# Performance work log

Hardware: AMD Instinct MI355X
Metric: run time of the kernel (lower is better)

The kernel has to match this reference:

```python
import jax, jax.numpy as jnp
import numpy as np

T = 4
TAU = 2.0
THR = 0.2
N_NODES = 50000
N_EDGES = 400000
N_LINKS = 50000
N_FEAT = 256
ENC0, ENC1 = 256, 128
DEC = 64


def _make_spike(grad_fn):
    @jax.custom_vjp
    def spike(v):
        return (v >= 0).astype(v.dtype)

    def fwd(v):
        return (v >= 0).astype(v.dtype), v

    def bwd(res, g):
        return (g * grad_fn(res),)

    spike.defvjp(fwd, bwd)
    return spike


def _sg_sigmoid(x, alpha=4.0):
    s = jax.nn.sigmoid(alpha * x)
    return alpha * s * (1.0 - s)


def _sg_pwl(x, w=0.5, c=0.0):
    return jnp.where(jnp.abs(x) < w, 1.0 / w, c)


spike_sig = _make_spike(_sg_sigmoid)   # default LIFNode surrogate (Sigmoid, alpha=4)
spike_pwl = _make_spike(_sg_pwl)       # PiecewiseLeakyReLU(w=0.5, c=0.0)


def _lif(v, x, spike_fn):
    # decay_input=False, v_reset=None -> soft reset, decay toward 0
    v = v * (1.0 - 1.0 / TAU) + x
    s = spike_fn(v - THR)
    return v - s * THR, s


def setup_inputs() -> dict:
    key = jax.random.key(0)
    ks = jax.random.split(key, 12)
    x = jax.random.uniform(ks[0], (N_NODES, N_FEAT), jnp.float32)
    edge_src = jax.random.randint(ks[1], (N_EDGES,), 0, N_NODES, jnp.int32)
    edge_dst = jax.random.randint(ks[2], (N_EDGES,), 0, N_NODES, jnp.int32)
    edge_w = jax.random.uniform(ks[3], (N_EDGES,), jnp.float32)
    nodes_s = jax.random.randint(ks[4], (N_LINKS,), 0, N_NODES, jnp.int32)
    nodes_t = jax.random.randint(ks[5], (N_LINKS,), 0, N_NODES, jnp.int32)
    W1 = jax.random.normal(ks[6], (N_FEAT, ENC0), jnp.float32) / np.sqrt(N_FEAT)
    W2 = jax.random.normal(ks[7], (N_FEAT + ENC0, ENC1), jnp.float32) / np.sqrt(N_FEAT + ENC0)
    Wd = jax.random.normal(ks[8], (ENC1, DEC), jnp.float32) / np.sqrt(ENC1)
    bd = jax.random.normal(ks[9], (DEC,), jnp.float32) * 0.01
    w_rec = jax.random.normal(ks[10], (DEC,), jnp.float32)
    return {"x": x, "W1": W1, "W2": W2, "Wd": Wd, "bd": bd, "w_rec": w_rec,
            "edge_w": edge_w, "edge_src": edge_src, "edge_dst": edge_dst,
            "nodes_s": nodes_s, "nodes_t": nodes_t}


def reference(x, W1, W2, Wd, bd, w_rec, edge_w, edge_src, edge_dst, nodes_s, nodes_t):
    N = x.shape[0]
    L = nodes_s.shape[0]
    key = jax.random.key(42)
    ew = edge_w[:, None]

    def propagate(feat):  # sparse adj @ feat via edge-list scatter-add
        return jax.ops.segment_sum(feat[edge_src] * ew, edge_dst, num_segments=N)

    def poisson(v, k):  # PoissonEncoder: spike ~ Bernoulli(v), zero gradient
        u = jax.random.uniform(k, v.shape, v.dtype)
        return (u <= jax.lax.stop_gradient(v)).astype(v.dtype)

    carry0 = (jnp.zeros((N, ENC0), x.dtype),              # v of layer0 z-LIF
              jnp.zeros((N, N_FEAT + ENC0), x.dtype),      # v of layer1 h-LIF
              jnp.zeros((N, ENC1), x.dtype),               # v of layer1 z-LIF
              jnp.zeros((2 * L, DEC), x.dtype))            # v of decoder LIF

    def step(carry, t):
        v0z, v1h, v1z, vdec = carry
        kt = jax.random.fold_in(key, t)
        k1, k2 = jax.random.split(kt)
        inp = poisson(x, k1)                    # inputs_encoding(x)
        h0 = propagate(inp)                     # layer0 GraphConvolution
        hs0 = poisson(h0, k2)                   # layer0 PoissonEncoder
        v0z, zs0 = _lif(v0z, hs0 @ W1, spike_pwl)
        inp1 = jnp.concatenate([zs0, hs0], axis=1)  # [N, 512]
        h1 = propagate(inp1)                    # layer1 GraphConvolution
        v1h, hs1 = _lif(v1h, h1, spike_sig)     # layer1 LIFNode (default surrogate)
        v1z, zs1 = _lif(v1z, hs1 @ W2, spike_pwl)
        hcat = jnp.concatenate([zs1[nodes_s], zs1[nodes_t]], axis=0)  # [2L, 128]
        vdec, zd = _lif(vdec, hcat @ Wd + bd, spike_pwl)
        y_t = jnp.sum(zd[:L] * w_rec * zd[L:], axis=1)  # WeightedInnerProduct_Link
        return (v0z, v1h, v1z, vdec), y_t

    _, y = jax.lax.scan(step, carry0, jnp.arange(T))  # y: [T, L]
    return jax.nn.sigmoid(jnp.mean(y, axis=0))        # PotentialOutput readout + sigmoid
```

## Files before the change

kernel.cpp:

```cpp
#include <hip/hip_runtime.h>
#include <stdint.h>
#include <math.h>

#define NN    50000
#define NE    400000
#define NL    50000
#define TOT   12800000

#define JAX_PARTITIONABLE 1

struct K8 { uint32_t a[4]; uint32_t b[4]; };

__host__ __device__ inline uint32_t rotl32(uint32_t x, int r){ return (x<<r)|(x>>(32-r)); }

__host__ __device__ inline void tf2x32(uint32_t k0, uint32_t k1, uint32_t x0, uint32_t x1,
                                       uint32_t &o0, uint32_t &o1) {
  uint32_t k2 = k0 ^ k1 ^ 0x1BD11BDAu;
  x0 += k0; x1 += k1;
#define TFR(r) { x0 += x1; x1 = rotl32(x1,(r)); x1 ^= x0; }
  TFR(13) TFR(15) TFR(26) TFR(6)
  x0 += k1; x1 += k2 + 1u;
  TFR(17) TFR(29) TFR(16) TFR(24)
  x0 += k2; x1 += k0 + 2u;
  TFR(13) TFR(15) TFR(26) TFR(6)
  x0 += k0; x1 += k1 + 3u;
  TFR(17) TFR(29) TFR(16) TFR(24)
  x0 += k1; x1 += k2 + 4u;
  TFR(13) TFR(15) TFR(26) TFR(6)
  x0 += k2; x1 += k0 + 5u;
#undef TFR
  o0 = x0; o1 = x1;
}

__device__ inline float u01(uint32_t b){
  return __uint_as_float((b>>9) | 0x3f800000u) - 1.0f;
}

__device__ inline uint32_t jax_bits32(uint32_t ka, uint32_t kb, uint32_t i, uint32_t total){
#if JAX_PARTITIONABLE
  uint32_t o0,o1; tf2x32(ka,kb, 0u, i, o0,o1); return o0^o1;
#else
  uint32_t h = total>>1; uint32_t o0,o1;
  if (i < h){ tf2x32(ka,kb, i, i+h, o0,o1); return o0; }
  else      { tf2x32(ka,kb, i-h, i, o0,o1); return o1; }
#endif
}

__device__ inline double shflxor_d(double x, int m){
  union { double d; int i[2]; } u; u.d = x;
  u.i[0] = __shfl_xor(u.i[0], m, 64);
  u.i[1] = __shfl_xor(u.i[1], m, 64);
  return u.d;
}

__device__ inline bool lif32(float &v, float a){
  v = __fadd_rn(__fmul_rn(v, 0.5f), a);
  float d = __fsub_rn(v, 0.2f);
  bool s = (d >= 0.0f);
  v = s ? d : v;
  return s;
}

#define FORCE_V(x) asm volatile("" : "+v"(x))

__device__ inline float bitmaskf(uint32_t w, int b, float wr){
#if __has_builtin(__builtin_amdgcn_sbfe)
  int m = __builtin_amdgcn_sbfe((int)w, b, 1);
#else
  int m = ((int)(w << (31-b))) >> 31;
#endif
  return __int_as_float(__float_as_int(wr) & m);
}

__global__ __launch_bounds__(256) void k_hist(const int* __restrict__ dst, int* __restrict__ cnt){
  int e = blockIdx.x*256 + threadIdx.x;
  if (e < NE) atomicAdd(&cnt[dst[e]], 1);
}

__global__ __launch_bounds__(1024) void k_scan(const int* __restrict__ cnt,
    int* __restrict__ rp, int* __restrict__ cur){
  __shared__ int buf[1024];
  __shared__ int carry;
  int tid = threadIdx.x;
  if (tid==0) carry = 0;
  __syncthreads();
  for (int base=0; base<NN; base+=1024){
    int v = (base+tid < NN) ? cnt[base+tid] : 0;
    buf[tid] = v; __syncthreads();
    for (int off=1; off<1024; off<<=1){
      int t = (tid>=off) ? buf[tid-off] : 0;
      __syncthreads();
      buf[tid] += t;
      __syncthreads();
    }
    int excl = buf[tid] - v + carry;
    if (base+tid < NN){ rp[base+tid] = excl; cur[base+tid] = excl; }
    __syncthreads();
    if (tid==0) carry += buf[1023];
    __syncthreads();
  }
  if (tid==0) rp[NN] = NE;
}

__global__ __launch_bounds__(256) void k_scatter(const int* __restrict__ dst,
    int* __restrict__ cur, int* __restrict__ eidx){
  int e = blockIdx.x*256 + threadIdx.x;
  if (e < NE){ int p = atomicAdd(&cur[dst[e]], 1); eidx[p] = e; }
}

__global__ __launch_bounds__(256) void k_sortrow(const int* __restrict__ rp,
    int* __restrict__ eidx, const int* __restrict__ esrc, const float* __restrict__ ew,
    int* __restrict__ csrc, float* __restrict__ cw){
  int n = blockIdx.x*256 + threadIdx.x;
  if (n >= NN) return;
  int lo = rp[n], hi = rp[n+1];
  for (int a=lo+1; a<hi; a++){
    int k = eidx[a]; int b = a-1;
    while (b>=lo && eidx[b]>k){ eidx[b+1]=eidx[b]; b--; }
    eidx[b+1] = k;
  }
  for (int p=lo; p<hi; p++){ int e = eidx[p]; csrc[p] = esrc[e]; cw[p] = ew[e]; }
}


__global__ __launch_bounds__(256) void k_pois_x(const float* __restrict__ x,
    uint64_t* __restrict__ bits, K8 K){
  int n = blockIdx.x, f = threadIdx.x;
  uint32_t i = (uint32_t)n*256u + (uint32_t)f;
  float xv = x[i];
  uint64_t pack[4];
  #pragma unroll
  for (int t=0;t<4;t++){
    bool b = (u01(jax_bits32(K.a[t],K.b[t], i, TOT)) <= xv);
    pack[t] = __ballot(b);
  }
  if ((f & 63)==0){
    uint64_t* dst = bits + ((size_t)n*4 + (f>>6))*4;
    #pragma unroll
    for (int t=0;t<4;t++) dst[t] = pack[t];
  }
}

__global__ __launch_bounds__(256) void k_h0(const int* __restrict__ rp,
    const int* __restrict__ csrc, const float* __restrict__ cw,
    const uint64_t* __restrict__ inb, uint64_t* __restrict__ outb, K8 K){
  int n = blockIdx.x, f = threadIdx.x;
  int wi = f>>6, sh = f&63;
  int lo = rp[n], hi = rp[n+1];
  float a[4] = {0.f,0.f,0.f,0.f};
  for (int p=lo;p<hi;p++){
    int s = csrc[p]; float w = cw[p];
    const uint64_t* bp = inb + ((size_t)s*4 + wi)*4;
    uint64_t w0=bp[0], w1=bp[1], w2=bp[2], w3=bp[3];
    a[0] = __fadd_rn(a[0], ((w0>>sh)&1ull) ? w : 0.0f);
    a[1] = __fadd_rn(a[1], ((w1>>sh)&1ull) ? w : 0.0f);
    a[2] = __fadd_rn(a[2], ((w2>>sh)&1ull) ? w : 0.0f);
    a[3] = __fadd_rn(a[3], ((w3>>sh)&1ull) ? w : 0.0f);
  }
  uint32_t i = (uint32_t)n*256u + (uint32_t)f;
  uint64_t pack[4];
  #pragma unroll
  for (int t=0;t<4;t++){
    bool b = (u01(jax_bits32(K.a[t],K.b[t], i, TOT)) <= a[t]);
    pack[t] = __ballot(b);
  }
  if (sh==0){
    uint64_t* dst = outb + ((size_t)n*4 + wi)*4;
    #pragma unroll
    for (int t=0;t<4;t++) dst[t] = pack[t];
  }
}

__global__ __launch_bounds__(256) void k_z0(const uint64_t* __restrict__ inb,
    const float* __restrict__ W, uint64_t* __restrict__ outb){
  __shared__ __align__(16) float sp[4*64*4];
  __shared__ uint64_t wbuf[16];
  int j = threadIdx.x;
  int n0 = blockIdx.x*4;
  float acc[4][4];
  #pragma unroll
  for (int t=0;t<4;t++)
    #pragma unroll
    for (int i=0;i<4;i++) acc[t][i] = 0.0f;

  for (int kt=0; kt<4; kt++){
    if (j < 16) wbuf[j] = inb[(((size_t)(n0+(j>>2)))*4 + kt)*4 + (j&3)];
    __syncthreads();
    {
      int i = j>>6, k = j&63;
      uint64_t w0=wbuf[i*4+0], w1=wbuf[i*4+1], w2=wbuf[i*4+2], w3=wbuf[i*4+3];
      float4 f;
      f.x = ((w0>>k)&1ull) ? 1.0f : 0.0f;
      f.y = ((w1>>k)&1ull) ? 1.0f : 0.0f;
      f.z = ((w2>>k)&1ull) ? 1.0f : 0.0f;
      f.w = ((w3>>k)&1ull) ? 1.0f : 0.0f;
      *(float4*)&sp[(i*64+k)*4] = f;
    }
    __syncthreads();
    const float* Wp = W + (size_t)(kt*64)*256 + j;
    #pragma unroll 4
    for (int q=0;q<64;q++){
      float wr = Wp[(size_t)q*256];
      float4 s0 = *(const float4*)&sp[(0*64+q)*4];
      float4 s1 = *(const float4*)&sp[(1*64+q)*4];
      float4 s2 = *(const float4*)&sp[(2*64+q)*4];
      float4 s3 = *(const float4*)&sp[(3*64+q)*4];
      acc[0][0]=__fmaf_rn(s0.x,wr,acc[0][0]); acc[1][0]=__fmaf_rn(s0.y,wr,acc[1][0]);
      acc[2][0]=__fmaf_rn(s0.z,wr,acc[2][0]); acc[3][0]=__fmaf_rn(s0.w,wr,acc[3][0]);
      acc[0][1]=__fmaf_rn(s1.x,wr,acc[0][1]); acc[1][1]=__fmaf_rn(s1.y,wr,acc[1][1]);
      acc[2][1]=__fmaf_rn(s1.z,wr,acc[2][1]); acc[3][1]=__fmaf_rn(s1.w,wr,acc[3][1]);
      acc[0][2]=__fmaf_rn(s2.x,wr,acc[0][2]); acc[1][2]=__fmaf_rn(s2.y,wr,acc[1][2]);
      acc[2][2]=__fmaf_rn(s2.z,wr,acc[2][2]); acc[3][2]=__fmaf_rn(s2.w,wr,acc[3][2]);
      acc[0][3]=__fmaf_rn(s3.x,wr,acc[0][3]); acc[1][3]=__fmaf_rn(s3.y,wr,acc[1][3]);
      acc[2][3]=__fmaf_rn(s3.z,wr,acc[2][3]); acc[3][3]=__fmaf_rn(s3.w,wr,acc[3][3]);
    }
    __syncthreads();
  }

  int wi = j>>6;
  #pragma unroll
  for (int i=0;i<4;i++){
    float v = 0.0f;
    uint64_t pack[4];
    #pragma unroll
    for (int t=0;t<4;t++){
      bool s = lif32(v, acc[t][i]);
      pack[t] = __ballot(s);
    }
    if ((j&63)==0){
      uint64_t* dst = outb + (((size_t)(n0+i))*4 + wi)*4;
      #pragma unroll
      for (int t=0;t<4;t++) dst[t] = pack[t];
    }
  }
}

__global__ __launch_bounds__(512) void k_h1(const int* __restrict__ rp,
    const int* __restrict__ csrc, const float* __restrict__ cw,
    const uint64_t* __restrict__ zs0b, const uint64_t* __restrict__ hs0b,
    uint64_t* __restrict__ hs1b){
  int n = blockIdx.x, f = threadIdx.x;
  int wi = f>>6, sh = f&63;
  const uint64_t* plane = (wi<4) ? zs0b : hs0b;
  int wo = wi & 3;
  int lo = rp[n], hi = rp[n+1];
  float a[4] = {0.f,0.f,0.f,0.f};
  for (int p=lo;p<hi;p++){
    int s = csrc[p]; float w = cw[p];
    const uint64_t* bp = plane + ((size_t)s*4 + wo)*4;
    uint64_t w0=bp[0], w1=bp[1], w2=bp[2], w3=bp[3];
    a[0] = __fadd_rn(a[0], ((w0>>sh)&1ull) ? w : 0.0f);
    a[1] = __fadd_rn(a[1], ((w1>>sh)&1ull) ? w : 0.0f);
    a[2] = __fadd_rn(a[2], ((w2>>sh)&1ull) ? w : 0.0f);
    a[3] = __fadd_rn(a[3], ((w3>>sh)&1ull) ? w : 0.0f);
  }
  float v = 0.0f;
  uint64_t pack[4];
  #pragma unroll
  for (int t=0;t<4;t++){
    bool s = lif32(v, a[t]);
    pack[t] = __ballot(s);
  }
  if (sh==0){
    uint64_t* dst = hs1b + ((size_t)n*8 + wi)*4;
    #pragma unroll
    for (int t=0;t<4;t++) dst[t] = pack[t];
  }
}

__global__ __launch_bounds__(128) void k_z1(const uint64_t* __restrict__ inb,
    const float* __restrict__ W, uint64_t* __restrict__ outb){
  __shared__ __align__(16) float sp[4*64*4];
  __shared__ uint64_t wbuf[16];
  int j = threadIdx.x;
  int n0 = blockIdx.x*4;
  float acc[4][4];
  #pragma unroll
  for (int t=0;t<4;t++)
    #pragma unroll
    for (int i=0;i<4;i++) acc[t][i] = 0.0f;

  for (int kt=0; kt<8; kt++){
    if (j < 16) wbuf[j] = inb[(((size_t)(n0+(j>>2)))*8 + kt)*4 + (j&3)];
    __syncthreads();
    #pragma unroll
    for (int rep=0; rep<2; rep++){
      int idx = rep*128 + j;
      int i = idx>>6, k = idx&63;
      uint64_t w0=wbuf[i*4+0], w1=wbuf[i*4+1], w2=wbuf[i*4+2], w3=wbuf[i*4+3];
      float4 f;
      f.x = ((w0>>k)&1ull) ? 1.0f : 0.0f;
      f.y = ((w1>>k)&1ull) ? 1.0f : 0.0f;
      f.z = ((w2>>k)&1ull) ? 1.0f : 0.0f;
      f.w = ((w3>>k)&1ull) ? 1.0f : 0.0f;
      *(float4*)&sp[(i*64+k)*4] = f;
    }
    __syncthreads();
    const float* Wp = W + (size_t)(kt*64)*128 + j;
    #pragma unroll 4
    for (int q=0;q<64;q++){
      float wr = Wp[(size_t)q*128];
      float4 s0 = *(const float4*)&sp[(0*64+q)*4];
      float4 s1 = *(const float4*)&sp[(1*64+q)*4];
      float4 s2 = *(const float4*)&sp[(2*64+q)*4];
      float4 s3 = *(const float4*)&sp[(3*64+q)*4];
      acc[0][0]=__fmaf_rn(s0.x,wr,acc[0][0]); acc[1][0]=__fmaf_rn(s0.y,wr,acc[1][0]);
      acc[2][0]=__fmaf_rn(s0.z,wr,acc[2][0]); acc[3][0]=__fmaf_rn(s0.w,wr,acc[3][0]);
      acc[0][1]=__fmaf_rn(s1.x,wr,acc[0][1]); acc[1][1]=__fmaf_rn(s1.y,wr,acc[1][1]);
      acc[2][1]=__fmaf_rn(s1.z,wr,acc[2][1]); acc[3][1]=__fmaf_rn(s1.w,wr,acc[3][1]);
      acc[0][2]=__fmaf_rn(s2.x,wr,acc[0][2]); acc[1][2]=__fmaf_rn(s2.y,wr,acc[1][2]);
      acc[2][2]=__fmaf_rn(s2.z,wr,acc[2][2]); acc[3][2]=__fmaf_rn(s2.w,wr,acc[3][2]);
      acc[0][3]=__fmaf_rn(s3.x,wr,acc[0][3]); acc[1][3]=__fmaf_rn(s3.y,wr,acc[1][3]);
      acc[2][3]=__fmaf_rn(s3.z,wr,acc[2][3]); acc[3][3]=__fmaf_rn(s3.w,wr,acc[3][3]);
    }
    __syncthreads();
  }

  int wi = j>>6;
  #pragma unroll
  for (int i=0;i<4;i++){
    float v = 0.0f;
    uint64_t pack[4];
    #pragma unroll
    for (int t=0;t<4;t++){
      bool s = lif32(v, acc[t][i]);
      pack[t] = __ballot(s);
    }
    if ((j&63)==0){
      uint64_t* dst = outb + (((size_t)(n0+i))*2 + wi)*4;
      #pragma unroll
      for (int t=0;t<4;t++) dst[t] = pack[t];
    }
  }
}

__global__ __launch_bounds__(128) void k_dec_y(const int* __restrict__ ns,
    const int* __restrict__ nt, const uint64_t* __restrict__ zs1b,
    const float* __restrict__ Wd, const float* __restrict__ bd,
    const float* __restrict__ wrec, float* __restrict__ out){
  int i = blockIdx.x;
  int tid = threadIdx.x;
  int row = tid>>6, j = tid&63;
  int node = row ? nt[i] : ns[i];
  float bdj = bd[j];
  double wrecj = (double)wrec[j];
  __shared__ uint64_t sw[2];

  uint32_t wlo[2][4], whi[2][4];
  const uint64_t* bp = zs1b + (size_t)node*8;
  #pragma unroll
  for (int g=0;g<2;g++)
    #pragma unroll
    for (int t=0;t<4;t++){
      uint64_t w8 = bp[g*4+t];
      wlo[g][t] = (uint32_t)w8;
      whi[g][t] = (uint32_t)(w8>>32);
      FORCE_V(wlo[g][t]); FORCE_V(whi[g][t]);
    }

  float acc[4] = {0.f,0.f,0.f,0.f};
  #pragma unroll
  for (int g=0;g<2;g++){
    #pragma unroll
    for (int h=0;h<2;h++){
      #pragma unroll
      for (int c=0;c<2;c++){
        float wr[16];
        #pragma unroll
        for (int q=0;q<16;q++) wr[q] = Wd[(size_t)(g*64+h*32+c*16+q)*64 + j];
        #pragma unroll
        for (int q=0;q<16;q++){
          int b = c*16+q;
          #pragma unroll
          for (int t=0;t<4;t++){
            uint32_t wv = h ? whi[g][t] : wlo[g][t];
            acc[t] = __fadd_rn(acc[t], bitmaskf(wv, b, wr[q]));
          }
        }
      }
    }
  }

  float v = 0.0f;
  double ysum = 0.0;
  #pragma unroll
  for (int t=0;t<4;t++){
    float a = __fadd_rn(acc[t], bdj);
    bool s = lif32(v, a);
    uint64_t bw = __ballot(s);
    if (j==0) sw[row] = bw;
    __syncthreads();
    uint64_t m = sw[0] & sw[1];
    __syncthreads();
    double term = ((m>>j)&1ull) ? wrecj : 0.0;
    #pragma unroll
    for (int off=1; off<64; off<<=1) term += shflxor_d(term, off);
    ysum += term;
  }
  if (tid==0) out[i] = (float)(1.0/(1.0 + exp(-0.25*ysum)));
}

extern "C" void kernel_launch(void* const* d_in, const int* in_sizes, int n_in,
                              void* d_out, int out_size, void* d_ws, size_t ws_size,
                              hipStream_t stream) {
  const float* x    = (const float*)d_in[0];
  const float* W1   = (const float*)d_in[1];
  const float* W2   = (const float*)d_in[2];
  const float* Wd   = (const float*)d_in[3];
  const float* bd   = (const float*)d_in[4];
  const float* wrec = (const float*)d_in[5];
  const float* ew   = (const float*)d_in[6];
  const int* esrc   = (const int*)d_in[7];
  const int* edst   = (const int*)d_in[8];
  const int* ns     = (const int*)d_in[9];
  const int* nt     = (const int*)d_in[10];
  float* out = (float*)d_out;
  (void)in_sizes; (void)n_in; (void)out_size; (void)ws_size;

  char* p = (char*)d_ws;
  uint64_t* inpb = (uint64_t*)p; p += (size_t)NN*16*8;
  uint64_t* hs0b = (uint64_t*)p; p += (size_t)NN*16*8;
  uint64_t* zs0b = (uint64_t*)p; p += (size_t)NN*16*8;
  uint64_t* hs1b = (uint64_t*)p; p += (size_t)NN*32*8;
  uint64_t* zs1b = (uint64_t*)p; p += (size_t)NN*8*8;
  int*   eidx = (int*)p;   p += (size_t)NE*4;
  int*   csrc = (int*)p;   p += (size_t)NE*4;
  float* cw   = (float*)p; p += (size_t)NE*4;
  int*   cnt  = (int*)p;   p += (size_t)(NN+2)*4;
  int*   rp   = (int*)p;   p += (size_t)(NN+2)*4;
  int*   cur  = (int*)p;   p += (size_t)(NN+2)*4;

  K8 K1, K2;
  for (int t=0;t<4;t++){
    uint32_t kt0,kt1;
    tf2x32(0u, 42u, 0u, (uint32_t)t, kt0, kt1);
#if JAX_PARTITIONABLE
    tf2x32(kt0, kt1, 0u, 0u, K1.a[t], K1.b[t]);
    tf2x32(kt0, kt1, 0u, 1u, K2.a[t], K2.b[t]);
#else
    uint32_t A0,B0,A1,B1;
    tf2x32(kt0, kt1, 0u, 2u, A0, B0);
    tf2x32(kt0, kt1, 1u, 3u, A1, B1);
    K1.a[t]=A0; K1.b[t]=A1; K2.a[t]=B0; K2.b[t]=B1;
#endif
  }

  hipMemsetAsync(cnt, 0, (size_t)NN*4, stream);
  k_hist   <<<(NE+255)/256, 256, 0, stream>>>(edst, cnt);
  k_scan   <<<1, 1024, 0, stream>>>(cnt, rp, cur);
  k_scatter<<<(NE+255)/256, 256, 0, stream>>>(edst, cur, eidx);
  k_sortrow<<<(NN+255)/256, 256, 0, stream>>>(rp, eidx, esrc, ew, csrc, cw);

  k_pois_x<<<NN, 256, 0, stream>>>(x, inpb, K1);
  k_h0    <<<NN, 256, 0, stream>>>(rp, csrc, cw, inpb, hs0b, K2);
  k_z0    <<<NN/4, 256, 0, stream>>>(hs0b, W1, zs0b);
  k_h1    <<<NN, 512, 0, stream>>>(rp, csrc, cw, zs0b, hs0b, hs1b);
  k_z1    <<<NN/4, 128, 0, stream>>>(hs1b, W2, zs1b);
  k_dec_y <<<NL, 128, 0, stream>>>(ns, nt, zs1b, Wd, bd, wrec, out);
}
```

Before: 1.739 ms.

## Retile z0/z1 spike GEMMs to eight nodes per block, two columns per thread

The dense spike-times-weight kernels now process eight nodes per block. Each thread computes two output columns for four nodes, so every LDS spike read feeds twice as many FMAs and each weight element is reused across more nodes. The staging step through a small shared word buffer, and the barrier that went with it, is removed: threads read packed bit-words straight from global memory when expanding them to floats. The cost is more accumulator registers per thread and half as many blocks.

Result: faster. 1.633 ms (-6.1%).

```diff
diff --git a/kernel.cpp b/kernel.cpp
--- a/kernel.cpp
+++ b/kernel.cpp
@@ -173,22 +173,26 @@
 
 __global__ __launch_bounds__(256) void k_z0(const uint64_t* __restrict__ inb,
     const float* __restrict__ W, uint64_t* __restrict__ outb){
-  __shared__ __align__(16) float sp[4*64*4];
-  __shared__ uint64_t wbuf[16];
-  int j = threadIdx.x;
-  int n0 = blockIdx.x*4;
-  float acc[4][4];
+  __shared__ __align__(16) float sp[8*64*4];
+  int tid = threadIdx.x;
+  int wave = tid>>6, lane = tid&63;
+  int g = wave>>1;
+  int ch = wave&1;
+  int colBase = ch*128;
+  int n0 = blockIdx.x*8;
+  float acc[4][4][2];
   #pragma unroll
   for (int t=0;t<4;t++)
     #pragma unroll
-    for (int i=0;i<4;i++) acc[t][i] = 0.0f;
+    for (int i=0;i<4;i++){ acc[t][i][0]=0.0f; acc[t][i][1]=0.0f; }
 
   for (int kt=0; kt<4; kt++){
-    if (j < 16) wbuf[j] = inb[(((size_t)(n0+(j>>2)))*4 + kt)*4 + (j&3)];
-    __syncthreads();
-    {
-      int i = j>>6, k = j&63;
-      uint64_t w0=wbuf[i*4+0], w1=wbuf[i*4+1], w2=wbuf[i*4+2], w3=wbuf[i*4+3];
+    #pragma unroll
+    for (int rep=0; rep<2; rep++){
+      int idx = rep*256 + tid;
+      int i = idx>>6, k = idx&63;
+      const uint64_t* bp = inb + (((size_t)(n0+i))*4 + kt)*4;
+      uint64_t w0=bp[0], w1=bp[1], w2=bp[2], w3=bp[3];
       float4 f;
       f.x = ((w0>>k)&1ull) ? 1.0f : 0.0f;
       f.y = ((w1>>k)&1ull) ? 1.0f : 0.0f;
@@ -197,40 +201,52 @@
       *(float4*)&sp[(i*64+k)*4] = f;
     }
     __syncthreads();
-    const float* Wp = W + (size_t)(kt*64)*256 + j;
+    const float* Wrow = W + (size_t)(kt*64)*256 + colBase + lane;
     #pragma unroll 4
     for (int q=0;q<64;q++){
-      float wr = Wp[(size_t)q*256];
-      float4 s0 = *(const float4*)&sp[(0*64+q)*4];
-      float4 s1 = *(const float4*)&sp[(1*64+q)*4];
-      float4 s2 = *(const float4*)&sp[(2*64+q)*4];
-      float4 s3 = *(const float4*)&sp[(3*64+q)*4];
-      acc[0][0]=__fmaf_rn(s0.x,wr,acc[0][0]); acc[1][0]=__fmaf_rn(s0.y,wr,acc[1][0]);
-      acc[2][0]=__fmaf_rn(s0.z,wr,acc[2][0]); acc[3][0]=__fmaf_rn(s0.w,wr,acc[3][0]);
-      acc[0][1]=__fmaf_rn(s1.x,wr,acc[0][1]); acc[1][1]=__fmaf_rn(s1.y,wr,acc[1][1]);
-      acc[2][1]=__fmaf_rn(s1.z,wr,acc[2][1]); acc[3][1]=__fmaf_rn(s1.w,wr,acc[3][1]);
-      acc[0][2]=__fmaf_rn(s2.x,wr,acc[0][2]); acc[1][2]=__fmaf_rn(s2.y,wr,acc[1][2]);
-      acc[2][2]=__fmaf_rn(s2.z,wr,acc[2][2]); acc[3][2]=__fmaf_rn(s2.w,wr,acc[3][2]);
-      acc[0][3]=__fmaf_rn(s3.x,wr,acc[0][3]); acc[1][3]=__fmaf_rn(s3.y,wr,acc[1][3]);
-      acc[2][3]=__fmaf_rn(s3.z,wr,acc[2][3]); acc[3][3]=__fmaf_rn(s3.w,wr,acc[3][3]);
-    }
-    __syncthreads();
-  }
-
-  int wi = j>>6;
+      float wr0 = Wrow[(size_t)q*256];
+      float wr1 = Wrow[(size_t)q*256 + 64];
+      float4 s0 = *(const float4*)&sp[((g*4+0)*64+q)*4];
+      float4 s1 = *(const float4*)&sp[((g*4+1)*64+q)*4];
+      float4 s2 = *(const float4*)&sp[((g*4+2)*64+q)*4];
+      float4 s3 = *(const float4*)&sp[((g*4+3)*64+q)*4];
+      acc[0][0][0]=__fmaf_rn(s0.x,wr0,acc[0][0][0]); acc[0][0][1]=__fmaf_rn(s0.x,wr1,acc[0][0][1]);
+      acc[1][0][0]=__fmaf_rn(s0.y,wr0,acc[1][0][0]); acc[1][0][1]=__fmaf_rn(s0.y,wr1,acc[1][0][1]);
+      acc[2][0][0]=__fmaf_rn(s0.z,wr0,acc[2][0][0]); acc[2][0][1]=__fmaf_rn(s0.z,wr1,acc[2][0][1]);
+      acc[3][0][0]=__fmaf_rn(s0.w,wr0,acc[3][0][0]); acc[3][0][1]=__fmaf_rn(s0.w,wr1,acc[3][0][1]);
+      acc[0][1][0]=__fmaf_rn(s1.x,wr0,acc[0][1][0]); acc[0][1][1]=__fmaf_rn(s1.x,wr1,acc[0][1][1]);
+      acc[1][1][0]=__fmaf_rn(s1.y,wr0,acc[1][1][0]); acc[1][1][1]=__fmaf_rn(s1.y,wr1,acc[1][1][1]);
+      acc[2][1][0]=__fmaf_rn(s1.z,wr0,acc[2][1][0]); acc[2][1][1]=__fmaf_rn(s1.z,wr1,acc[2][1][1]);
+      acc[3][1][0]=__fmaf_rn(s1.w,wr0,acc[3][1][0]); acc[3][1][1]=__fmaf_rn(s1.w,wr1,acc[3][1][1]);
+      acc[0][2][0]=__fmaf_rn(s2.x,wr0,acc[0][2][0]); acc[0][2][1]=__fmaf_rn(s2.x,wr1,acc[0][2][1]);
+      acc[1][2][0]=__fmaf_rn(s2.y,wr0,acc[1][2][0]); acc[1][2][1]=__fmaf_rn(s2.y,wr1,acc[1][2][1]);
+      acc[2][2][0]=__fmaf_rn(s2.z,wr0,acc[2][2][0]); acc[2][2][1]=__fmaf_rn(s2.z,wr1,acc[2][2][1]);
+      acc[3][2][0]=__fmaf_rn(s2.w,wr0,acc[3][2][0]); acc[3][2][1]=__fmaf_rn(s2.w,wr1,acc[3][2][1]);
+      acc[0][3][0]=__fmaf_rn(s3.x,wr0,acc[0][3][0]); acc[0][3][1]=__fmaf_rn(s3.x,wr1,acc[0][3][1]);
+      acc[1][3][0]=__fmaf_rn(s3.y,wr0,acc[1][3][0]); acc[1][3][1]=__fmaf_rn(s3.y,wr1,acc[1][3][1]);
+      acc[2][3][0]=__fmaf_rn(s3.z,wr0,acc[2][3][0]); acc[2][3][1]=__fmaf_rn(s3.z,wr1,acc[2][3][1]);
+      acc[3][3][0]=__fmaf_rn(s3.w,wr0,acc[3][3][0]); acc[3][3][1]=__fmaf_rn(s3.w,wr1,acc[3][3][1]);
+    }
+    __syncthreads();
+  }
+
   #pragma unroll
   for (int i=0;i<4;i++){
-    float v = 0.0f;
-    uint64_t pack[4];
+    int node = n0 + g*4 + i;
+    float v0 = 0.0f, v1 = 0.0f;
+    uint64_t p0[4], p1[4];
     #pragma unroll
     for (int t=0;t<4;t++){
-      bool s = lif32(v, acc[t][i]);
-      pack[t] = __ballot(s);
-    }
-    if ((j&63)==0){
-      uint64_t* dst = outb + (((size_t)(n0+i))*4 + wi)*4;
+      bool s0 = lif32(v0, acc[t][i][0]);
+      bool s1 = lif32(v1, acc[t][i][1]);
+      p0[t] = __ballot(s0);
+      p1[t] = __ballot(s1);
+    }
+    if (lane==0){
+      uint64_t* d0 = outb + ((size_t)node*4 + ch*2    )*4;
+      uint64_t* d1 = outb + ((size_t)node*4 + ch*2 + 1)*4;
       #pragma unroll
-      for (int t=0;t<4;t++) dst[t] = pack[t];
+      for (int t=0;t<4;t++){ d0[t]=p0[t]; d1[t]=p1[t]; }
     }
   }
 }
@@ -270,24 +286,23 @@
 
 __global__ __launch_bounds__(128) void k_z1(const uint64_t* __restrict__ inb,
     const float* __restrict__ W, uint64_t* __restrict__ outb){
-  __shared__ __align__(16) float sp[4*64*4];
-  __shared__ uint64_t wbuf[16];
-  int j = threadIdx.x;
-  int n0 = blockIdx.x*4;
-  float acc[4][4];
+  __shared__ __align__(16) float sp[8*64*4];
+  int tid = threadIdx.x;
+  int g = tid>>6, lane = tid&63;
+  int n0 = blockIdx.x*8;
+  float acc[4][4][2];
   #pragma unroll
   for (int t=0;t<4;t++)
     #pragma unroll
-    for (int i=0;i<4;i++) acc[t][i] = 0.0f;
+    for (int i=0;i<4;i++){ acc[t][i][0]=0.0f; acc[t][i][1]=0.0f; }
 
   for (int kt=0; kt<8; kt++){
-    if (j < 16) wbuf[j] = inb[(((size_t)(n0+(j>>2)))*8 + kt)*4 + (j&3)];
-    __syncthreads();
-    #pragma unroll
-    for (int rep=0; rep<2; rep++){
-      int idx = rep*128 + j;
+    #pragma unroll
+    for (int rep=0; rep<4; rep++){
+      int idx = rep*128 + tid;
       int i = idx>>6, k = idx&63;
-      uint64_t w0=wbuf[i*4+0], w1=wbuf[i*4+1], w2=wbuf[i*4+2], w3=wbuf[i*4+3];
+      const uint64_t* bp = inb + (((size_t)(n0+i))*8 + kt)*4;
+      uint64_t w0=bp[0], w1=bp[1], w2=bp[2], w3=bp[3];
       float4 f;
       f.x = ((w0>>k)&1ull) ? 1.0f : 0.0f;
       f.y = ((w1>>k)&1ull) ? 1.0f : 0.0f;
@@ -296,40 +311,52 @@
       *(float4*)&sp[(i*64+k)*4] = f;
     }
     __syncthreads();
-    const float* Wp = W + (size_t)(kt*64)*128 + j;
+    const float* Wrow = W + (size_t)(kt*64)*128 + lane;
     #pragma unroll 4
     for (int q=0;q<64;q++){
-      float wr = Wp[(size_t)q*128];
-      float4 s0 = *(const float4*)&sp[(0*64+q)*4];
-      float4 s1 = *(const float4*)&sp[(1*64+q)*4];
-      float4 s2 = *(const float4*)&sp[(2*64+q)*4];
-      float4 s3 = *(const float4*)&sp[(3*64+q)*4];
-      acc[0][0]=__fmaf_rn(s0.x,wr,acc[0][0]); acc[1][0]=__fmaf_rn(s0.y,wr,acc[1][0]);
-      acc[2][0]=__fmaf_rn(s0.z,wr,acc[2][0]); acc[3][0]=__fmaf_rn(s0.w,wr,acc[3][0]);
-      acc[0][1]=__fmaf_rn(s1.x,wr,acc[0][1]); acc[1][1]=__fmaf_rn(s1.y,wr,acc[1][1]);
-      acc[2][1]=__fmaf_rn(s1.z,wr,acc[2][1]); acc[3][1]=__fmaf_rn(s1.w,wr,acc[3][1]);
-      acc[0][2]=__fmaf_rn(s2.x,wr,acc[0][2]); acc[1][2]=__fmaf_rn(s2.y,wr,acc[1][2]);
-      acc[2][2]=__fmaf_rn(s2.z,wr,acc[2][2]); acc[3][2]=__fmaf_rn(s2.w,wr,acc[3][2]);
-      acc[0][3]=__fmaf_rn(s3.x,wr,acc[0][3]); acc[1][3]=__fmaf_rn(s3.y,wr,acc[1][3]);
-      acc[2][3]=__fmaf_rn(s3.z,wr,acc[2][3]); acc[3][3]=__fmaf_rn(s3.w,wr,acc[3][3]);
-    }
-    __syncthreads();
-  }
-
-  int wi = j>>6;
+      float wr0 = Wrow[(size_t)q*128];
+      float wr1 = Wrow[(size_t)q*128 + 64];
+      float4 s0 = *(const float4*)&sp[((g*4+0)*64+q)*4];
+      float4 s1 = *(const float4*)&sp[((g*4+1)*64+q)*4];
+      float4 s2 = *(const float4*)&sp[((g*4+2)*64+q)*4];
+      float4 s3 = *(const float4*)&sp[((g*4+3)*64+q)*4];
+      acc[0][0][0]=__fmaf_rn(s0.x,wr0,acc[0][0][0]); acc[0][0][1]=__fmaf_rn(s0.x,wr1,acc[0][0][1]);
+      acc[1][0][0]=__fmaf_rn(s0.y,wr0,acc[1][0][0]); acc[1][0][1]=__fmaf_rn(s0.y,wr1,acc[1][0][1]);
+      acc[2][0][0]=__fmaf_rn(s0.z,wr0,acc[2][0][0]); acc[2][0][1]=__fmaf_rn(s0.z,wr1,acc[2][0][1]);
+      acc[3][0][0]=__fmaf_rn(s0.w,wr0,acc[3][0][0]); acc[3][0][1]=__fmaf_rn(s0.w,wr1,acc[3][0][1]);
+      acc[0][1][0]=__fmaf_rn(s1.x,wr0,acc[0][1][0]); acc[0][1][1]=__fmaf_rn(s1.x,wr1,acc[0][1][1]);
+      acc[1][1][0]=__fmaf_rn(s1.y,wr0,acc[1][1][0]); acc[1][1][1]=__fmaf_rn(s1.y,wr1,acc[1][1][1]);
+      acc[2][1][0]=__fmaf_rn(s1.z,wr0,acc[2][1][0]); acc[2][1][1]=__fmaf_rn(s1.z,wr1,acc[2][1][1]);
+      acc[3][1][0]=__fmaf_rn(s1.w,wr0,acc[3][1][0]); acc[3][1][1]=__fmaf_rn(s1.w,wr1,acc[3][1][1]);
+      acc[0][2][0]=__fmaf_rn(s2.x,wr0,acc[0][2][0]); acc[0][2][1]=__fmaf_rn(s2.x,wr1,acc[0][2][1]);
+      acc[1][2][0]=__fmaf_rn(s2.y,wr0,acc[1][2][0]); acc[1][2][1]=__fmaf_rn(s2.y,wr1,acc[1][2][1]);
+      acc[2][2][0]=__fmaf_rn(s2.z,wr0,acc[2][2][0]); acc[2][2][1]=__fmaf_rn(s2.z,wr1,acc[2][2][1]);
+      acc[3][2][0]=__fmaf_rn(s2.w,wr0,acc[3][2][0]); acc[3][2][1]=__fmaf_rn(s2.w,wr1,acc[3][2][1]);
+      acc[0][3][0]=__fmaf_rn(s3.x,wr0,acc[0][3][0]); acc[0][3][1]=__fmaf_rn(s3.x,wr1,acc[0][3][1]);
+      acc[1][3][0]=__fmaf_rn(s3.y,wr0,acc[1][3][0]); acc[1][3][1]=__fmaf_rn(s3.y,wr1,acc[1][3][1]);
+      acc[2][3][0]=__fmaf_rn(s3.z,wr0,acc[2][3][0]); acc[2][3][1]=__fmaf_rn(s3.z,wr1,acc[2][3][1]);
+      acc[3][3][0]=__fmaf_rn(s3.w,wr0,acc[3][3][0]); acc[3][3][1]=__fmaf_rn(s3.w,wr1,acc[3][3][1]);
+    }
+    __syncthreads();
+  }
+
   #pragma unroll
   for (int i=0;i<4;i++){
-    float v = 0.0f;
-    uint64_t pack[4];
+    int node = n0 + g*4 + i;
+    float v0 = 0.0f, v1 = 0.0f;
+    uint64_t p0[4], p1[4];
     #pragma unroll
     for (int t=0;t<4;t++){
-      bool s = lif32(v, acc[t][i]);
-      pack[t] = __ballot(s);
-    }
-    if ((j&63)==0){
-      uint64_t* dst = outb + (((size_t)(n0+i))*2 + wi)*4;
+      bool s0 = lif32(v0, acc[t][i][0]);
+      bool s1 = lif32(v1, acc[t][i][1]);
+      p0[t] = __ballot(s0);
+      p1[t] = __ballot(s1);
+    }
+    if (lane==0){
+      uint64_t* d0 = outb + ((size_t)node*2 + 0)*4;
+      uint64_t* d1 = outb + ((size_t)node*2 + 1)*4;
       #pragma unroll
-      for (int t=0;t<4;t++) dst[t] = pack[t];
+      for (int t=0;t<4;t++){ d0[t]=p0[t]; d1[t]=p1[t]; }
     }
   }
 }
@@ -453,8 +480,8 @@
 
   k_pois_x<<<NN, 256, 0, stream>>>(x, inpb, K1);
   k_h0    <<<NN, 256, 0, stream>>>(rp, csrc, cw, inpb, hs0b, K2);
-  k_z0    <<<NN/4, 256, 0, stream>>>(hs0b, W1, zs0b);
+  k_z0    <<<NN/8, 256, 0, stream>>>(hs0b, W1, zs0b);
   k_h1    <<<NN, 512, 0, stream>>>(rp, csrc, cw, zs0b, hs0b, hs1b);
-  k_z1    <<<NN/4, 128, 0, stream>>>(hs1b, W2, zs1b);
+  k_z1    <<<NN/8, 128, 0, stream>>>(hs1b, W2, zs1b);
   k_dec_y <<<NL, 128, 0, stream>>>(ns, nt, zs1b, Wd, bd, wrec, out);
 }
```
